# Kernel tuning notes

Hardware: AMD Instinct MI355X
Metric: run time of the kernel (lower is better)

The kernel has to match this reference:

```python
import jax, jax.numpy as jnp
import numpy as np

EPS = 1e-8  # torch CosineSimilarity default eps

def _normalize(x):
    # torch clamps each norm at eps before dividing
    n = jnp.sqrt(jnp.sum(x * x, axis=-1, keepdims=True))
    return x / jnp.maximum(n, EPS)

def _cross_entropy(logits, labels):
    logp = jax.nn.log_softmax(logits, axis=-1)
    return -jnp.mean(jnp.take_along_axis(logp, labels[:, None], axis=-1))

def setup_inputs() -> dict:
    key = jax.random.key(0)
    ks = jax.random.split(key, 7)
    B, M, D = 8192, 3129, 512
    return {
        'mm_proj': jax.random.normal(ks[0], (B, D), jnp.float32),
        'ans_embedding': jax.random.normal(ks[1], (M, D), jnp.float32),
        'v_max': jax.random.normal(ks[2], (B, D), jnp.float32),
        'mm': jax.random.normal(ks[3], (B, D), jnp.float32),
        'logits_q': jax.random.normal(ks[4], (B, M), jnp.float32),
        'logits_rubi': jax.random.normal(ks[5], (B, M), jnp.float32),
        'class_id': jax.random.randint(ks[6], (B, 1), 0, M, jnp.int64),
    }

def reference(mm_proj, ans_embedding, v_max, mm, logits_q, logits_rubi, class_id,
              question_loss_weight=1.0):
    cid = class_id.squeeze(1)  # [B]
    # NCE over cosine similarities: fuse normalize + GEMM instead of [B,M,D] expand
    g = _normalize(mm_proj)          # [B, D]
    a = _normalize(ans_embedding)    # [M, D]
    d_logit = jnp.einsum('bd,md->bm', g, a)  # [B, M] cosine matrix
    positive_dist = jnp.take_along_axis(d_logit, cid[:, None], axis=1)[:, 0]  # [B]
    num = jnp.exp(positive_dist)
    den = jnp.sum(jnp.exp(d_logit), axis=-1)
    loss_nce = jnp.mean(-jnp.log(num / den))
    # object cosine loss
    obj_dist = jnp.sum(_normalize(v_max) * _normalize(mm), axis=-1)  # [B]
    obj_loss = jnp.mean(1.0 - obj_dist)
    fusion_loss = (_cross_entropy(logits_rubi, cid) + obj_loss + loss_nce) / 3.0
    question_loss = _cross_entropy(logits_q, cid)
    loss = fusion_loss + question_loss_weight * question_loss
    # out['loss'], out['loss_mm_q'], out['loss_q']
    return jnp.stack([loss, fusion_loss, question_loss])
```

## Files before the change

### kernel.cpp

```cpp
#include <hip/hip_runtime.h>
#include <hip/hip_bf16.h>

#define B_N 8192
#define M_N 3129
#define M_PAD 3200
#define D_N 512

#define CE_WPA 100128
#define CE_WTOT (2 * CE_WPA)
#define CE_WAVES 8344
#define CE_BLOCKS 2086

#define GLOBAL_AS __attribute__((address_space(1)))
#define LDS_AS __attribute__((address_space(3)))

typedef __bf16 bf16x8 __attribute__((ext_vector_type(8)));
typedef float f32x4 __attribute__((ext_vector_type(4)));

#define PREP_G_BLOCKS   (B_N / 4)
#define PREP_A_BLOCKS   (M_PAD / 4)
#define PREP_OBJ_BLOCKS (B_N / 4)

__device__ __forceinline__ void normalize_row(
    const float* __restrict__ x, __bf16* __restrict__ y,
    int row, int nrows_src, int lane) {
  bf16x8 out;
  if (row >= nrows_src) {
    for (int j = 0; j < 8; ++j) out[j] = (__bf16)0.0f;
    *(bf16x8*)(y + (size_t)row * D_N + lane * 8) = out;
    return;
  }
  const float4* xr = (const float4*)(x + (size_t)row * D_N);
  float4 v0 = xr[lane * 2], v1 = xr[lane * 2 + 1];
  float s = v0.x*v0.x + v0.y*v0.y + v0.z*v0.z + v0.w*v0.w
          + v1.x*v1.x + v1.y*v1.y + v1.z*v1.z + v1.w*v1.w;
  for (int o = 1; o < 64; o <<= 1) s += __shfl_xor(s, o);
  float rn = 1.0f / fmaxf(sqrtf(s), 1e-8f);
  float vals[8] = {v0.x, v0.y, v0.z, v0.w, v1.x, v1.y, v1.z, v1.w};
  for (int j = 0; j < 8; ++j) out[j] = (__bf16)(vals[j] * rn);
  *(bf16x8*)(y + (size_t)row * D_N + lane * 8) = out;
}

__global__ __launch_bounds__(256) void prep_kernel(
    const float* __restrict__ mm_proj, const float* __restrict__ ans_emb,
    const float* __restrict__ v_max, const float* __restrict__ mm,
    __bf16* __restrict__ g, __bf16* __restrict__ a,
    float* __restrict__ obj) {
  int blk = blockIdx.x;
  int wid = threadIdx.x >> 6, lane = threadIdx.x & 63;
  if (blk < PREP_G_BLOCKS) {
    normalize_row(mm_proj, g, blk * 4 + wid, B_N, lane);
  } else if (blk < PREP_G_BLOCKS + PREP_A_BLOCKS) {
    normalize_row(ans_emb, a, (blk - PREP_G_BLOCKS) * 4 + wid, M_N, lane);
  } else {
    int b = (blk - PREP_G_BLOCKS - PREP_A_BLOCKS) * 4 + wid;
    const float4* vr = (const float4*)(v_max + (size_t)b * D_N);
    const float4* mr = (const float4*)(mm + (size_t)b * D_N);
    float4 a0 = vr[lane * 2], a1 = vr[lane * 2 + 1];
    float4 b0 = mr[lane * 2], b1 = mr[lane * 2 + 1];
    float sv = a0.x*a0.x + a0.y*a0.y + a0.z*a0.z + a0.w*a0.w
             + a1.x*a1.x + a1.y*a1.y + a1.z*a1.z + a1.w*a1.w;
    float sm = b0.x*b0.x + b0.y*b0.y + b0.z*b0.z + b0.w*b0.w
             + b1.x*b1.x + b1.y*b1.y + b1.z*b1.z + b1.w*b1.w;
    float sd = a0.x*b0.x + a0.y*b0.y + a0.z*b0.z + a0.w*b0.w
             + a1.x*b1.x + a1.y*b1.y + a1.z*b1.z + a1.w*b1.w;
    for (int o = 1; o < 64; o <<= 1) {
      sv += __shfl_xor(sv, o);
      sm += __shfl_xor(sm, o);
      sd += __shfl_xor(sd, o);
    }
    if (lane == 0) {
      float dist = sd / (fmaxf(sqrtf(sv), 1e-8f) * fmaxf(sqrtf(sm), 1e-8f));
      obj[b] = 1.0f - dist;
    }
  }
}

__global__ __launch_bounds__(256) void pos_kernel(
    const __bf16* __restrict__ g, const __bf16* __restrict__ a,
    const int* __restrict__ cid, float* __restrict__ pos) {
  int wid = threadIdx.x >> 6, lane = threadIdx.x & 63;
  int b = blockIdx.x * 4 + wid;
  if (b >= B_N) return;
  int label = cid[b];
  bf16x8 gv = *(const bf16x8*)(g + (size_t)b * D_N + lane * 8);
  bf16x8 av = *(const bf16x8*)(a + (size_t)label * D_N + lane * 8);
  float s = 0.0f;
  for (int j = 0; j < 8; ++j) s += (float)gv[j] * (float)av[j];
  for (int o = 1; o < 64; o <<= 1) s += __shfl_xor(s, o);
  if (lane == 0) pos[b] = s;
}

__global__ __launch_bounds__(256) void nce_gemm_kernel(
    const __bf16* __restrict__ g, const __bf16* __restrict__ a,
    float* __restrict__ den) {
  __shared__ __bf16 As[128 * 32];
  __shared__ __bf16 Bs[128 * 32];
  const int t = threadIdx.x;
  const int brow0 = blockIdx.y * 128;
  const int mrow0 = blockIdx.x * 128;
  const int lane = t & 63;
  const int wid = t >> 6;
  const int wrow = wid >> 1;
  const int wcol = wid & 1;
  const int r = lane & 15;
  const int quad = lane >> 4;

  f32x4 acc[4][4];
  for (int i = 0; i < 4; ++i)
    for (int j = 0; j < 4; ++j)
      acc[i][j] = f32x4{0.f, 0.f, 0.f, 0.f};

  for (int k0 = 0; k0 < D_N; k0 += 32) {
    __syncthreads();
    for (int i = 0; i < 2; ++i) {
      int s = t + i * 256;
      int row = s >> 2;
      int kq = (s & 3) << 3;
      const __bf16* ga = g + (size_t)(brow0 + row) * D_N + (k0 + kq);
      __builtin_amdgcn_global_load_lds((const GLOBAL_AS void*)ga,
                                       (LDS_AS void*)(As + s * 8), 16, 0, 0);
      const __bf16* gb = a + (size_t)(mrow0 + row) * D_N + (k0 + kq);
      __builtin_amdgcn_global_load_lds((const GLOBAL_AS void*)gb,
                                       (LDS_AS void*)(Bs + s * 8), 16, 0, 0);
    }
    __syncthreads();
    bf16x8 af[4], bf[4];
    for (int i = 0; i < 4; ++i)
      af[i] = *(const bf16x8*)(As + (wrow * 64 + i * 16 + r) * 32 + quad * 8);
    for (int j = 0; j < 4; ++j)
      bf[j] = *(const bf16x8*)(Bs + (wcol * 64 + j * 16 + r) * 32 + quad * 8);
    for (int i = 0; i < 4; ++i)
      for (int j = 0; j < 4; ++j)
        acc[i][j] = __builtin_amdgcn_mfma_f32_16x16x32_bf16(af[i], bf[j],
                                                            acc[i][j], 0, 0, 0);
  }

  for (int i = 0; i < 4; ++i) {
    for (int reg = 0; reg < 4; ++reg) {
      float s = 0.0f;
      for (int j = 0; j < 4; ++j) {
        int m = mrow0 + wcol * 64 + j * 16 + r;
        if (m < M_N) s += __expf(acc[i][j][reg]);
      }
      s += __shfl_xor(s, 1);
      s += __shfl_xor(s, 2);
      s += __shfl_xor(s, 4);
      s += __shfl_xor(s, 8);
      if (r == 0) {
        int b = brow0 + wrow * 64 + i * 16 + quad * 4 + reg;
        atomicAdd(den + b, s);
      }
    }
  }
}

__global__ __launch_bounds__(256) void ce_sum_kernel(
    const float* __restrict__ lq, const float* __restrict__ lr,
    float* __restrict__ rowsum) {
  const int lane = threadIdx.x & 63;
  const int gw = (int)((blockIdx.x * 256 + threadIdx.x) >> 6);
#pragma unroll 1
  for (int gidx = 0; gidx < 6; ++gidx) {
    float4 v[4];
    unsigned e0[4];
    int arr[4];
#pragma unroll
    for (int k = 0; k < 4; ++k) {
      int w = gw + (gidx * 4 + k) * CE_WAVES;
      int aidx = (w >= CE_WPA) ? 1 : 0;
      unsigned chunk = (unsigned)(w - aidx * CE_WPA) * 64u + (unsigned)lane;
      e0[k] = chunk * 4u;
      arr[k] = aidx;
      const float* base = aidx ? lr : lq;
      v[k] = *(const float4*)(base + (size_t)chunk * 4u);
    }
#pragma unroll
    for (int k = 0; k < 4; ++k) {
      unsigned row0 = e0[k] / M_N;
      unsigned bound = (row0 + 1u) * M_N;
      float ex0 = __expf(v[k].x), ex1 = __expf(v[k].y),
            ex2 = __expf(v[k].z), ex3 = __expf(v[k].w);
      float s_lo = 0.f, s_hi = 0.f;
      if (e0[k] + 0u < bound) s_lo += ex0; else s_hi += ex0;
      if (e0[k] + 1u < bound) s_lo += ex1; else s_hi += ex1;
      if (e0[k] + 2u < bound) s_lo += ex2; else s_hi += ex2;
      if (e0[k] + 3u < bound) s_lo += ex3; else s_hi += ex3;
      unsigned rA = (unsigned)__builtin_amdgcn_readfirstlane((int)row0);
      float cA = (row0 == rA) ? s_lo : 0.f;
      float cB = (row0 == rA) ? s_hi : s_lo;
      for (int o = 1; o < 64; o <<= 1) {
        cA += __shfl_xor(cA, o);
        cB += __shfl_xor(cB, o);
      }
      if (lane == 0) {
        float* rs = rowsum + (arr[k] ? B_N : 0);
        atomicAdd(rs + rA, cA);
        if (cB != 0.f) atomicAdd(rs + rA + 1, cB);
      }
    }
  }
}

__global__ __launch_bounds__(256) void final_reduce_kernel(
    const float* __restrict__ den, const float* __restrict__ pos,
    const float* __restrict__ rowsum,
    const float* __restrict__ lq, const float* __restrict__ lr,
    const int* __restrict__ cid, const float* __restrict__ obj,
    float* __restrict__ acc) {
  int b = blockIdx.x * 256 + threadIdx.x;
  int lab = cid[b];
  float xq = lq[(size_t)b * M_N + lab];
  float xr = lr[(size_t)b * M_N + lab];
  float s_nce = logf(den[b]) - pos[b];
  float s_ceq = logf(rowsum[b]) - xq;
  float s_cer = logf(rowsum[B_N + b]) - xr;
  float s_obj = obj[b];
  for (int o = 1; o < 64; o <<= 1) {
    s_nce += __shfl_xor(s_nce, o);
    s_ceq += __shfl_xor(s_ceq, o);
    s_cer += __shfl_xor(s_cer, o);
    s_obj += __shfl_xor(s_obj, o);
  }
  __shared__ float red[4][4];
  int wid = threadIdx.x >> 6;
  if ((threadIdx.x & 63) == 0) {
    red[wid][0] = s_nce; red[wid][1] = s_ceq;
    red[wid][2] = s_cer; red[wid][3] = s_obj;
  }
  __syncthreads();
  if (threadIdx.x < 4) {
    float v = red[0][threadIdx.x] + red[1][threadIdx.x]
            + red[2][threadIdx.x] + red[3][threadIdx.x];
    atomicAdd(acc + threadIdx.x, v);
  }
}

__global__ void final_combine_kernel(const float* __restrict__ acc,
                                     float* __restrict__ out) {
  if (threadIdx.x == 0) {
    float nce = acc[0] / (float)B_N;
    float ceq = acc[1] / (float)B_N;
    float cer = acc[2] / (float)B_N;
    float ob  = acc[3] / (float)B_N;
    float fusion = (cer + ob + nce) * (1.0f / 3.0f);
    out[0] = fusion + ceq;
    out[1] = fusion;
    out[2] = ceq;
  }
}

extern "C" void kernel_launch(void* const* d_in, const int* in_sizes, int n_in,
                              void* d_out, int out_size, void* d_ws, size_t ws_size,
                              hipStream_t stream) {
  const float* mm_proj     = (const float*)d_in[0];
  const float* ans_emb     = (const float*)d_in[1];
  const float* v_max       = (const float*)d_in[2];
  const float* mm          = (const float*)d_in[3];
  const float* logits_q    = (const float*)d_in[4];
  const float* logits_rubi = (const float*)d_in[5];
  const int*   cid         = (const int*)d_in[6];
  float* out = (float*)d_out;

  char* ws = (char*)d_ws;
  __bf16* g = (__bf16*)ws;
  __bf16* a = (__bf16*)(ws + 8388608);
  float* den    = (float*)(ws + 8388608 + 3276800);
  float* rowsum = den + B_N;
  float* acc    = rowsum + 2 * B_N;
  float* pos    = acc + 4;
  float* obj    = pos + B_N;

  hipMemsetAsync(den, 0, (size_t)(3 * B_N + 4) * sizeof(float), stream);

  prep_kernel<<<PREP_G_BLOCKS + PREP_A_BLOCKS + PREP_OBJ_BLOCKS, 256, 0,
                stream>>>(mm_proj, ans_emb, v_max, mm, g, a, obj);
  pos_kernel<<<B_N / 4, 256, 0, stream>>>(g, a, cid, pos);
  nce_gemm_kernel<<<dim3(M_PAD / 128, B_N / 128), 256, 0, stream>>>(g, a, den);
  ce_sum_kernel<<<CE_BLOCKS, 256, 0, stream>>>(logits_q, logits_rubi, rowsum);
  final_reduce_kernel<<<B_N / 256, 256, 0, stream>>>(den, pos, rowsum,
                                                     logits_q, logits_rubi,
                                                     cid, obj, acc);
  final_combine_kernel<<<1, 64, 0, stream>>>(acc, out);
}
```

Baseline: 338.4 us.

## Give each CE wave a contiguous 3072-element span with one reduction and atomic

The cross-entropy row-sum kernel now gives each wave a contiguous span of 12 float4 chunks per lane. Previously each wave reduced 24 strided 256-element chunks, each needing its own cross-lane shuffle reduction and atomics. The new loop accumulates exp sums in registers with a 6-deep rolling prefetch buffer and does one shuffle reduction and at most two atomics per wave. This relies on CE_SPAN (3072) being smaller than the row length (3129), so each span crosses at most one row boundary. It also cuts the grid-wide shuffle and atomic traffic.

After: 329.7 us. -2.6%, faster.

```diff
diff --git a/kernel.cpp b/kernel.cpp
--- a/kernel.cpp
+++ b/kernel.cpp
@@ -6,10 +6,11 @@
 #define M_PAD 3200
 #define D_N 512
 
-#define CE_WPA 100128
+#define CE_L 12
+#define CE_SPAN (CE_L * 256)
+#define CE_WPA 8344
 #define CE_WTOT (2 * CE_WPA)
-#define CE_WAVES 8344
-#define CE_BLOCKS 2086
+#define CE_BLOCKS (CE_WTOT / 4)
 
 #define GLOBAL_AS __attribute__((address_space(1)))
 #define LDS_AS __attribute__((address_space(3)))
@@ -160,45 +161,41 @@
     float* __restrict__ rowsum) {
   const int lane = threadIdx.x & 63;
   const int gw = (int)((blockIdx.x * 256 + threadIdx.x) >> 6);
-#pragma unroll 1
-  for (int gidx = 0; gidx < 6; ++gidx) {
-    float4 v[4];
-    unsigned e0[4];
-    int arr[4];
+  const int aidx = (gw >= CE_WPA) ? 1 : 0;
+  const unsigned wl = (unsigned)(gw - aidx * CE_WPA);
+  const unsigned f0 = wl * (unsigned)CE_SPAN;
+  const unsigned r0 = f0 / (unsigned)M_N;
+  const unsigned b1 = (r0 + 1u) * (unsigned)M_N;
+  const float* base = aidx ? lr : lq;
+  const float* p = base + f0 + (unsigned)lane * 4u;
+
+  float4 buf[6];
 #pragma unroll
-    for (int k = 0; k < 4; ++k) {
-      int w = gw + (gidx * 4 + k) * CE_WAVES;
-      int aidx = (w >= CE_WPA) ? 1 : 0;
-      unsigned chunk = (unsigned)(w - aidx * CE_WPA) * 64u + (unsigned)lane;
-      e0[k] = chunk * 4u;
-      arr[k] = aidx;
-      const float* base = aidx ? lr : lq;
-      v[k] = *(const float4*)(base + (size_t)chunk * 4u);
-    }
+  for (int i = 0; i < 6; ++i) buf[i] = *(const float4*)(p + i * 256);
+
+  float a0 = 0.f, a1 = 0.f;
+  const unsigned fbase = f0 + (unsigned)lane * 4u;
 #pragma unroll
-    for (int k = 0; k < 4; ++k) {
-      unsigned row0 = e0[k] / M_N;
-      unsigned bound = (row0 + 1u) * M_N;
-      float ex0 = __expf(v[k].x), ex1 = __expf(v[k].y),
-            ex2 = __expf(v[k].z), ex3 = __expf(v[k].w);
-      float s_lo = 0.f, s_hi = 0.f;
-      if (e0[k] + 0u < bound) s_lo += ex0; else s_hi += ex0;
-      if (e0[k] + 1u < bound) s_lo += ex1; else s_hi += ex1;
-      if (e0[k] + 2u < bound) s_lo += ex2; else s_hi += ex2;
-      if (e0[k] + 3u < bound) s_lo += ex3; else s_hi += ex3;
-      unsigned rA = (unsigned)__builtin_amdgcn_readfirstlane((int)row0);
-      float cA = (row0 == rA) ? s_lo : 0.f;
-      float cB = (row0 == rA) ? s_hi : s_lo;
-      for (int o = 1; o < 64; o <<= 1) {
-        cA += __shfl_xor(cA, o);
-        cB += __shfl_xor(cB, o);
-      }
-      if (lane == 0) {
-        float* rs = rowsum + (arr[k] ? B_N : 0);
-        atomicAdd(rs + rA, cA);
-        if (cB != 0.f) atomicAdd(rs + rA + 1, cB);
-      }
-    }
+  for (int i = 0; i < CE_L; ++i) {
+    float4 v = buf[i % 6];
+    if (i + 6 < CE_L) buf[i % 6] = *(const float4*)(p + (i + 6) * 256);
+    unsigned f = fbase + (unsigned)i * 256u;
+    float e0 = __expf(v.x), e1 = __expf(v.y), e2 = __expf(v.z), e3 = __expf(v.w);
+    float lo = 0.f, hi = 0.f;
+    if (f + 0u < b1) lo += e0; else hi += e0;
+    if (f + 1u < b1) lo += e1; else hi += e1;
+    if (f + 2u < b1) lo += e2; else hi += e2;
+    if (f + 3u < b1) lo += e3; else hi += e3;
+    a0 += lo; a1 += hi;
+  }
+  for (int o = 1; o < 64; o <<= 1) {
+    a0 += __shfl_xor(a0, o);
+    a1 += __shfl_xor(a1, o);
+  }
+  if (lane == 0) {
+    float* rs = rowsum + (aidx ? B_N : 0);
+    atomicAdd(rs + r0, a0);
+    if (a1 != 0.f) atomicAdd(rs + r0 + 1, a1);
   }
 }
 
```
